# Kernel tuning notes

Hardware: AMD Instinct MI355X
Metric: run time of the kernel (lower is better)

## Reference

```python
import jax, jax.numpy as jnp
import numpy as np
from jax import lax

GROUPS = 32
CH = 2048
CG = CH // GROUPS  # 64 channels per group
H = W = 64
B = 4
EPS = 1e-5


def _conv2d(x, w, b, padding, dilation=1):
    # x: [N, Cin, H, W], w: [Cout, Cin, kh, kw] (OIHW)
    y = lax.conv_general_dilated(
        x, w, window_strides=(1, 1),
        padding=[(padding, padding), (padding, padding)],
        rhs_dilation=(dilation, dilation),
        dimension_numbers=("NCHW", "OIHW", "NCHW"))
    return y + b[None, :, None, None]


def _prelu(x, alpha):
    # single shared slope (num_parameters=1)
    return jnp.where(x >= 0, x, alpha[0] * x)


def setup_inputs() -> dict:
    key = jax.random.key(0)
    ks = jax.random.split(key, 6)
    s = 0.05
    f32 = jnp.float32
    return {
        "x": jax.random.normal(ks[0], (B, CH, H, W), f32),
        # EFFM.conv1x1 (on concatenated pooled h/w strips)
        "w_hw": jax.random.normal(ks[1], (CG, CG, 1, 1), f32) * s,
        "b_hw": jnp.zeros((CG,), f32),
        # GroupNorm(cg, cg): per-channel affine
        "gn_w": jnp.ones((CG,), f32),
        "gn_b": jnp.zeros((CG,), f32),
        # RC branch1: 3x3 conv pad=1 + PReLU
        "w_b1": jax.random.normal(ks[2], (CG, CG, 3, 3), f32) * s,
        "b_b1": jnp.zeros((CG,), f32),
        "a_b1": jnp.full((1,), 0.25, f32),
        # RC branch2: 3x3 conv dilation=2 pad=2 + PReLU
        "w_b2": jax.random.normal(ks[3], (CG, CG, 3, 3), f32) * s,
        "b_b2": jnp.zeros((CG,), f32),
        "a_b2": jnp.full((1,), 0.25, f32),
        # RC conv128to64: 1x1 conv 2*cg -> cg
        "w_cat": jax.random.normal(ks[4], (CG, 2 * CG, 1, 1), f32) * s,
        "b_cat": jnp.zeros((CG,), f32),
    }


def _effm(x, w_hw, b_hw, gn_w, gn_b, w_b1, b_b1, a_b1, w_b2, b_b2, a_b2, w_cat, b_cat):
    b, c, h, w = x.shape
    cg = c // GROUPS
    bg = b * GROUPS
    gx = x.reshape(bg, cg, h, w)

    # --- coordinate attention branch ---
    x_h = jnp.mean(gx, axis=3, keepdims=True)                       # [bg, cg, h, 1]
    x_w = jnp.mean(gx, axis=2, keepdims=True).transpose(0, 1, 3, 2)  # [bg, cg, w, 1]
    hw = jnp.concatenate([x_h, x_w], axis=2)                         # [bg, cg, h+w, 1]
    # 1x1 conv == channel mixing linear
    hw = jnp.einsum("oi,bilk->bolk", w_hw[:, :, 0, 0], hw) + b_hw[None, :, None, None]
    x_h, x_w = hw[:, :, :h, :], hw[:, :, h:, :]
    gate = gx * jax.nn.sigmoid(x_h) * jax.nn.sigmoid(x_w.transpose(0, 1, 3, 2))

    # GroupNorm(num_groups=cg, num_channels=cg) == per-channel instance norm
    mu = jnp.mean(gate, axis=(2, 3), keepdims=True)
    var = jnp.var(gate, axis=(2, 3), keepdims=True)
    x1 = (gate - mu) * lax.rsqrt(var + EPS)
    x1 = x1 * gn_w[None, :, None, None] + gn_b[None, :, None, None]

    # --- RC multi-scale branch ---
    br1 = _prelu(_conv2d(gx, w_b1, b_b1, padding=1), a_b1) + gx
    br2 = _prelu(_conv2d(gx, w_b2, b_b2, padding=2, dilation=2), a_b2) + gx
    cat = jnp.concatenate([br1, br2], axis=1)                        # [bg, 2cg, h, w]
    x2 = jnp.einsum("oi,bihw->bohw", w_cat[:, :, 0, 0], cat) + b_cat[None, :, None, None]

    # --- cross softmax-matmul attention ---
    x11 = jax.nn.softmax(jnp.mean(x1, axis=(2, 3)), axis=-1)          # [bg, cg]
    x21 = jax.nn.softmax(jnp.mean(x2, axis=(2, 3)), axis=-1)          # [bg, cg]
    weights = (jnp.einsum("gc,gchw->ghw", x11, x2)
               + jnp.einsum("gc,gchw->ghw", x21, x1))                # [bg, h, w]
    out = gx * jax.nn.sigmoid(weights)[:, None, :, :]
    return out.reshape(b, c, h, w)


def reference(x, w_hw, b_hw, gn_w, gn_b, w_b1, b_b1, a_b1, w_b2, b_b2, a_b2, w_cat, b_cat):
    return _effm(x, w_hw, b_hw, gn_w, gn_b, w_b1, b_b1, a_b1, w_b2, b_b2, a_b2, w_cat, b_cat)
```

## Files before the change

### kernel.cpp

```cpp
#include <hip/hip_runtime.h>
#include <hip/hip_bf16.h>

#define HWPX 4096

typedef __attribute__((ext_vector_type(8))) short short8v;
typedef __attribute__((ext_vector_type(4))) float f32x4;
typedef __attribute__((ext_vector_type(16))) float f32x16;
#define MFMA32(a,b,c) __builtin_amdgcn_mfma_f32_32x32x16_bf16(a,b,c,0,0,0)

__device__ __forceinline__ float sigf(float x){ return 1.0f/(1.0f+__expf(-x)); }
__device__ __forceinline__ unsigned short f2bf(float f){
  __hip_bfloat16 h = __float2bfloat16(f);
  unsigned short u; __builtin_memcpy(&u, &h, sizeof(u)); return u;
}
__device__ __forceinline__ float bf2f(unsigned short u){
  return __uint_as_float(((unsigned)u)<<16);
}
__device__ __forceinline__ void gl2lds16(const void* g, void* l){
  __builtin_amdgcn_global_load_lds((const __attribute__((address_space(1))) void*)g,
                                   (__attribute__((address_space(3))) void*)l, 16, 0, 0);
}

__global__ __launch_bounds__(256) void k_prep(const float* wb1, const float* wb2,
                                              const float* wcat, const float* gnb,
                                              unsigned short* wimg, unsigned short* wcimg,
                                              float* x11){
  int bid = blockIdx.x, tid = threadIdx.x;
  for (int idx = bid*256 + tid; idx < 73728; idx += 64*256){
    int f = idx >> 9, r = idx & 511, lane = r >> 3, j = r & 7;
    int qc = f / 36, rem = f % 36, tap = rem >> 2, kc = rem & 3;
    int q = qc >> 1, conv = qc & 1, kf = kc >> 1, cot = kc & 1;
    int co = cot*32 + (lane & 31);
    int ci = q*32 + kf*16 + (lane >> 5)*8 + j;
    const float* src = conv ? wb2 : wb1;
    wimg[idx] = f2bf(src[(co*64 + ci)*9 + tap]);
  }
  if (bid == 0){
    for (int idx = tid; idx < 8192; idx += 256){
      int f = idx >> 9, r = idx & 511, lane = r >> 3, j = r & 7;
      int kfc = f >> 1, cot = f & 1;
      int o = cot*32 + (lane & 31);
      int ch = kfc*16 + (lane >> 5)*8 + j;
      wcimg[idx] = f2bf(wcat[o*128 + ch]);
    }
    if (tid < 64){
      float g = gnb[tid];
      float m = g;
      for (int s=32; s; s>>=1) m = fmaxf(m, __shfl_xor(m, s));
      float e = __expf(g-m);
      float se = e;
      for (int s=32; s; s>>=1) se += __shfl_xor(se, s);
      x11[tid] = e/se;
    }
  }
}

__global__ __launch_bounds__(256) void k_rc(const float* __restrict__ x,
                                            unsigned short* __restrict__ xb,
                                            float* __restrict__ hwbuf){
  int blk = blockIdx.x;
  int g = blk >> 3, slot = blk & 7;
  int tid = threadIdx.x;
  int col = tid & 63, wid = tid >> 6;
  __shared__ float rsm[8*64];
  __shared__ float csm[4*8*64];
  float colacc[8] = {0,0,0,0,0,0,0,0};
  const float* xbase = x + ((size_t)(g*64 + slot*8))*HWPX;
  for (int p=0;p<16;++p){
    int r = wid + 4*p;
    const float* src = xbase + r*64 + col;
    float v[8];
    #pragma unroll
    for (int e=0;e<8;e++) v[e] = src[(size_t)e*HWPX];
    unsigned pk[4];
    #pragma unroll
    for (int j=0;j<4;j++) pk[j] = (unsigned)f2bf(v[2*j]) | ((unsigned)f2bf(v[2*j+1])<<16);
    f32x4 st; __builtin_memcpy(&st, pk, 16);
    *(f32x4*)((char*)xb + (((size_t)(g*64+r))*8 + slot)*1024 + col*16) = st;
    #pragma unroll
    for (int e=0;e<8;e++){
      float s = v[e];
      s += __shfl_xor(s,1); s += __shfl_xor(s,2); s += __shfl_xor(s,4);
      s += __shfl_xor(s,8); s += __shfl_xor(s,16); s += __shfl_xor(s,32);
      if ((tid&63)==0) rsm[e*64+r] = s;
      colacc[e] += v[e];
    }
  }
  #pragma unroll
  for (int e=0;e<8;e++) csm[(wid*8+e)*64+col] = colacc[e];
  __syncthreads();
  float* hb = hwbuf + ((size_t)(g*64 + slot*8))*128;
  for (int idx=tid; idx<512; idx+=256){
    int e = idx>>6, r = idx&63;
    hb[e*128 + r] = rsm[e*64+r] * (1.0f/64.0f);
  }
  for (int idx=tid; idx<512; idx+=256){
    int e = idx>>6, c2 = idx&63;
    float s = csm[(0*8+e)*64+c2] + csm[(1*8+e)*64+c2] + csm[(2*8+e)*64+c2] + csm[(3*8+e)*64+c2];
    hb[e*128 + 64 + c2] = s * (1.0f/64.0f);
  }
}

__global__ __launch_bounds__(256) void k_hwmm(const float* hwbuf, const float* whw,
                                              const float* bhw, float* sigbuf){
  int g = blockIdx.x;
  __shared__ float hl[64*128];
  int tid = threadIdx.x;
  const float* src = hwbuf + (size_t)g*8192;
  for (int i = tid; i < 2048; i += 256) ((float4*)hl)[i] = ((const float4*)src)[i];
  __syncthreads();
  int p  = tid & 127;
  int o0 = (tid >> 7) * 32;
  float acc[32];
  #pragma unroll
  for (int k=0;k<32;k++) acc[k] = bhw[o0+k];
  for (int i=0;i<64;i++){
    float v = hl[i*128+p];
    #pragma unroll
    for (int k=0;k<32;k++) acc[k] = fmaf(whw[(o0+k)*64+i], v, acc[k]);
  }
  float* dst = sigbuf + (size_t)g*8192;
  #pragma unroll
  for (int k=0;k<32;k++) dst[(o0+k)*128+p] = sigf(acc[k]);
}

__global__ __launch_bounds__(256) void k_gate2(const unsigned short* __restrict__ xb,
                                               const float* __restrict__ sigbuf,
                                               const float* __restrict__ gnw,
                                               const float* __restrict__ gnb,
                                               float* __restrict__ scsh){
  int blk = blockIdx.x;
  int g = blk >> 3, slot = blk & 7;
  int tid = threadIdx.x, col = tid & 63, wq = tid >> 6, lane = tid & 63;
  __shared__ float srm[8*64], scm[8*64], red[4*16];
  for (int idx = tid; idx < 1024; idx += 256){
    int e = idx >> 7, k = idx & 127;
    float v = sigbuf[(size_t)g*8192 + (size_t)(slot*8+e)*128 + k];
    if (k < 64) srm[e*64+k] = v; else scm[e*64+k-64] = v;
  }
  __syncthreads();
  float s[8] = {0,0,0,0,0,0,0,0}, s2[8] = {0,0,0,0,0,0,0,0};
  const char* base = (const char*)xb + (((size_t)(g*64))*8 + slot)*1024;
  for (int p=0;p<16;++p){
    int row = wq*16 + p;
    short8v xv = *(const short8v*)(base + (size_t)row*8192 + col*16);
    #pragma unroll
    for (int e=0;e<8;e++){
      float v = bf2f((unsigned short)xv[e]) * srm[e*64+row] * scm[e*64+col];
      s[e] += v; s2[e] = fmaf(v, v, s2[e]);
    }
  }
  #pragma unroll
  for (int e=0;e<8;e++){
    #pragma unroll
    for (int off=1; off<64; off<<=1){ s[e] += __shfl_xor(s[e], off); s2[e] += __shfl_xor(s2[e], off); }
  }
  if (lane == 0){
    #pragma unroll
    for (int e=0;e<8;e++){ red[wq*16+e] = s[e]; red[wq*16+8+e] = s2[e]; }
  }
  __syncthreads();
  if (tid < 8){
    float S  = red[tid]   + red[16+tid] + red[32+tid] + red[48+tid];
    float S2 = red[8+tid] + red[24+tid] + red[40+tid] + red[56+tid];
    float mu = S*(1.f/4096.f);
    float var = S2*(1.f/4096.f) - mu*mu;
    int c = slot*8 + tid;
    float scale = rsqrtf(var + 1e-5f) * gnw[c];
    scsh[(g*64+c)*2]   = scale;
    scsh[(g*64+c)*2+1] = gnb[c] - mu*scale;
  }
}

__global__ __launch_bounds__(512) void k_convcat(const unsigned short* __restrict__ xb,
                                                 const char* __restrict__ wgl,
                                                 const char* __restrict__ wcgl,
                                                 const float* __restrict__ bb1,
                                                 const float* __restrict__ bb2,
                                                 const float* __restrict__ a1p,
                                                 const float* __restrict__ a2p,
                                                 const float* __restrict__ bcat,
                                                 const float* __restrict__ x11,
                                                 float* __restrict__ wsum2,
                                                 float* __restrict__ x2mean){
  extern __shared__ char smem[];
  char* INL = smem;
  char* WL  = smem + 52224;
  char* BRL = smem;
  char* WCL = smem + 131072;
  float* x11l = (float*)(smem + 147456);
  float* bcl  = x11l + 64;

  const int tid = threadIdx.x;
  const int g = blockIdx.x >> 3;
  const int strip = blockIdx.x & 7;
  const int r0 = strip*8;
  const int w = tid >> 6;
  const int lane = tid & 63;
  const int l31 = lane & 31;
  const int lh  = lane >> 5;
  const int conv = w >> 2;
  const int ch2 = (w >> 1) & 1;
  const int rquad = w & 1;
  const int dil = conv + 1;

  #pragma unroll
  for (int k=0;k<2;k++){
    int idx = tid + k*512;
    gl2lds16(wcgl + (size_t)idx*16, WCL + idx*16);
  }
  if (tid < 64){ x11l[tid] = x11[tid]; bcl[tid] = bcat[tid]; }
  if (tid < 192){
    int seg = tid >> 2, pc = tid & 3;
    int colp = (pc < 2) ? pc : pc + 64;
    *(f32x4*)(INL + seg*1088 + colp*16) = (f32x4){0.f,0.f,0.f,0.f};
  }

  f32x16 acc[2][4];
  #pragma unroll
  for (int cot=0;cot<2;cot++)
    #pragma unroll
    for (int pt=0;pt<4;pt++)
      #pragma unroll
      for (int e=0;e<16;e++) acc[cot][pt][e] = 0.f;

  const float alpha = conv ? a2p[0] : a1p[0];
  const float* bbp = conv ? bb2 : bb1;

  for (int q=0;q<2;++q){
    if (q) __syncthreads();
    #pragma unroll
    for (int k=0;k<9;k++){
      int idx = tid + k*512;
      gl2lds16(wgl + (size_t)q*73728 + (size_t)idx*16, WL + idx*16);
    }
    #pragma unroll
    for (int i=0;i<6;++i){
      int seg = w*6 + i;
      int row = seg >> 2, slot = seg & 3;
      int rg = r0 - 2 + row;
      char* dst = INL + seg*1088 + 32;
      if ((unsigned)rg < 64u){
        const char* src = (const char*)xb + ((((size_t)(g*64+rg))*8) + q*4 + slot)*1024 + lane*16;
        gl2lds16(src, dst + lane*16);
      } else {
        *(f32x4*)(dst + lane*16) = (f32x4){0.f,0.f,0.f,0.f};
      }
    }
    __syncthreads();
    #pragma unroll
    for (int tap=0;tap<9;++tap){
      const int dy = tap/3 - 1, dx = tap%3 - 1;
      #pragma unroll
      for (int kf=0;kf<2;++kf){
        const char* wp = WL + (size_t)(((conv*9+tap)*4 + kf*2)*1024) + lane*16;
        short8v A0 = *(const short8v*)(wp);
        short8v A1 = *(const short8v*)(wp + 1024);
        const char* ib = INL + (kf*2 + lh)*1088 + (ch2*32 + 2 + l31 + dx*dil)*16;
        #pragma unroll
        for (int pt=0;pt<4;++pt){
          int rowin = rquad*4 + pt + dy*dil + 2;
          short8v B = *(const short8v*)(ib + rowin*4352);
          acc[0][pt] = MFMA32(A0, B, acc[0][pt]);
          acc[1][pt] = MFMA32(A1, B, acc[1][pt]);
        }
      }
    }
  }
  __syncthreads();

  #pragma unroll
  for (int cot=0;cot<2;++cot){
    #pragma unroll
    for (int rq=0;rq<4;++rq){
      int co0 = cot*32 + 8*rq + 4*lh;
      float b0 = bbp[co0], b1 = bbp[co0+1], b2 = bbp[co0+2], b3 = bbp[co0+3];
      int ch0 = conv*64 + co0;
      #pragma unroll
      for (int pt=0;pt<4;++pt){
        int prow = rquad*4 + pt;
        int colg = ch2*32 + l31;
        const char* rsrc = (const char*)xb + (((size_t)(g*64 + r0 + prow))*8 + (co0>>3))*1024
                           + colg*16 + (co0&7)*2;
        ushort4 rv = *(const ushort4*)rsrc;
        float v0 = acc[cot][pt][rq*4+0] + b0; v0 = (v0>=0.f? v0 : alpha*v0) + bf2f(rv.x);
        float v1 = acc[cot][pt][rq*4+1] + b1; v1 = (v1>=0.f? v1 : alpha*v1) + bf2f(rv.y);
        float v2 = acc[cot][pt][rq*4+2] + b2; v2 = (v2>=0.f? v2 : alpha*v2) + bf2f(rv.z);
        float v3 = acc[cot][pt][rq*4+3] + b3; v3 = (v3>=0.f? v3 : alpha*v3) + bf2f(rv.w);
        int px = prow*64 + colg;
        int addr = (px*256 + ch0*2) ^ ((px & 15) << 4);
        ushort4 pk; pk.x=f2bf(v0); pk.y=f2bf(v1); pk.z=f2bf(v2); pk.w=f2bf(v3);
        *(ushort4*)(BRL + addr) = pk;
      }
    }
  }
  __syncthreads();

  {
    f32x16 c2[2][2];
    #pragma unroll
    for (int cot=0;cot<2;cot++)
      #pragma unroll
      for (int t=0;t<2;t++)
        #pragma unroll
        for (int e=0;e<16;e++) c2[cot][t][e] = 0.f;

    #pragma unroll
    for (int kfc=0;kfc<8;++kfc){
      const char* ap = WCL + (size_t)(kfc*2*1024) + lane*16;
      short8v A0 = *(const short8v*)(ap);
      short8v A1 = *(const short8v*)(ap + 1024);
      #pragma unroll
      for (int t=0;t<2;++t){
        int px = w*64 + t*32 + l31;
        int addr = (px*256 + kfc*32 + lh*16) ^ ((px & 15) << 4);
        short8v B = *(const short8v*)(BRL + addr);
        c2[0][t] = MFMA32(A0, B, c2[0][t]);
        c2[1][t] = MFMA32(A1, B, c2[1][t]);
      }
    }
    float u0 = 0.f, u1 = 0.f;
    #pragma unroll
    for (int cot=0;cot<2;++cot){
      #pragma unroll
      for (int reg=0;reg<16;++reg){
        int o = cot*32 + (reg&3) + 8*(reg>>2) + 4*lh;
        float xw = x11l[o], bc = bcl[o];
        u0 += xw*(c2[cot][0][reg] + bc);
        u1 += xw*(c2[cot][1][reg] + bc);
        float sv = c2[cot][0][reg] + c2[cot][1][reg];
        sv += __shfl_xor(sv, 1); sv += __shfl_xor(sv, 2);
        sv += __shfl_xor(sv, 4); sv += __shfl_xor(sv, 8); sv += __shfl_xor(sv, 16);
        if (l31 == 0) atomicAdd(&x2mean[g*64 + o], sv);
      }
    }
    u0 += __shfl_xor(u0, 32);
    u1 += __shfl_xor(u1, 32);
    if (lh == 0){
      float* wp2 = wsum2 + (size_t)g*4096 + strip*512 + w*64 + l31;
      wp2[0]  = u0;
      wp2[32] = u1;
    }
  }
}

__global__ __launch_bounds__(64) void k_x21s(const float* x2mean, const float* bcat, float* x21){
  int g = blockIdx.x;
  int o = threadIdx.x;
  float mean = x2mean[g*64 + o] * (1.f/4096.f) + bcat[o];
  float mx = mean;
  for (int s=32; s; s>>=1) mx = fmaxf(mx, __shfl_xor(mx, s));
  float e = __expf(mean - mx);
  float se = e;
  for (int s=32; s; s>>=1) se += __shfl_xor(se, s);
  x21[g*64 + o] = e/se;
}

__global__ __launch_bounds__(256) void k_final(const float* __restrict__ x,
                                               const float* __restrict__ sigbuf,
                                               const float* __restrict__ scsh,
                                               const float* __restrict__ x21,
                                               const float* __restrict__ wsum2,
                                               float* __restrict__ out){
  int blk = blockIdx.x;
  int g = blk >> 4, chunk = blk & 15;
  int tid = threadIdx.x;
  __shared__ float crow[64*4];
  __shared__ float ccol[64*64];
  __shared__ float Ssm;
  const float* sgb = sigbuf + (size_t)g*8192;
  {
    int c = tid >> 2, rr = tid & 3;
    crow[tid] = x21[g*64+c] * scsh[(g*64+c)*2] * sgb[c*128 + chunk*4 + rr];
  }
  for (int idx = tid; idx < 4096; idx += 256){
    int c = idx >> 6, col = idx & 63;
    ccol[idx] = sgb[c*128 + 64 + col];
  }
  if (tid < 64){
    float v = x21[g*64+tid] * scsh[(g*64+tid)*2+1];
    for (int s=32; s; s>>=1) v += __shfl_xor(v, s);
    if (tid == 0) Ssm = v;
  }
  __syncthreads();
  int px = chunk*256 + tid;
  int rr = tid >> 6, col = tid & 63;
  const float* xp = x + (size_t)(g*64)*HWPX + px;
  float W = wsum2[(size_t)g*4096 + px] + Ssm;
  #pragma unroll 4
  for (int c=0;c<64;c++){
    W = fmaf(crow[c*4+rr]*ccol[c*64+col], xp[(size_t)c*HWPX], W);
  }
  float s = sigf(W);
  float* op = out + (size_t)(g*64)*HWPX + px;
  #pragma unroll 4
  for (int c=0;c<64;c++){
    op[(size_t)c*HWPX] = xp[(size_t)c*HWPX] * s;
  }
}

extern "C" void kernel_launch(void* const* d_in, const int* in_sizes, int n_in,
                              void* d_out, int out_size, void* d_ws, size_t ws_size,
                              hipStream_t stream) {
  const float* x     = (const float*)d_in[0];
  const float* w_hw  = (const float*)d_in[1];
  const float* b_hw  = (const float*)d_in[2];
  const float* gn_w  = (const float*)d_in[3];
  const float* gn_b  = (const float*)d_in[4];
  const float* w_b1  = (const float*)d_in[5];
  const float* b_b1  = (const float*)d_in[6];
  const float* a_b1  = (const float*)d_in[7];
  const float* w_b2  = (const float*)d_in[8];
  const float* b_b2  = (const float*)d_in[9];
  const float* a_b2  = (const float*)d_in[10];
  const float* w_cat = (const float*)d_in[11];
  const float* b_cat = (const float*)d_in[12];

  char* ws = (char*)d_ws;
  unsigned short* wimg  = (unsigned short*)(ws + 0);
  unsigned short* wcimg = (unsigned short*)(ws + 147456);
  float* x11    = (float*)(ws + 163840);
  float* x21    = (float*)(ws + 164096);
  float* x2mean = (float*)(ws + 196864);
  float* scsh   = (float*)(ws + 229632);
  float* wsum2  = (float*)(ws + 295168);
  float* hwbuf  = (float*)(ws + 2392320);
  float* sigb   = (float*)(ws + 6586624);
  unsigned short* xb = (unsigned short*)d_out;
  float* out = (float*)d_out;

  hipFuncSetAttribute(reinterpret_cast<const void*>(k_convcat),
                      hipFuncAttributeMaxDynamicSharedMemorySize, 147968);

  k_prep <<<64,   256, 0, stream>>>(w_b1, w_b2, w_cat, gn_b, wimg, wcimg, x11);
  k_rc   <<<1024, 256, 0, stream>>>(x, xb, hwbuf);
  k_hwmm <<<128,  256, 0, stream>>>(hwbuf, w_hw, b_hw, sigb);
  k_gate2<<<1024, 256, 0, stream>>>(xb, sigb, gn_w, gn_b, scsh);
  hipMemsetAsync(x2mean, 0, 32768, stream);
  k_convcat<<<1024, 512, 147968, stream>>>(xb, (const char*)wimg, (const char*)wcimg,
                                           b_b1, b_b2, a_b1, a_b2, b_cat, x11, wsum2, x2mean);
  k_x21s <<<128,  64, 0, stream>>>(x2mean, b_cat, x21);
  k_final<<<2048, 256, 0, stream>>>(x, sigb, scsh, x21, wsum2, out);
}
```

Baseline: 298.4 us.

## Merge prep/rc/memset launches, restructure convcat staging, fuse x21 softmax into final

The weight-prep, x-cast/pooling and x2mean zeroing kernels are folded into one launch, and the x21 softmax kernel is folded into the final kernel, removing several launches and a memset. In convcat, the per-half weight staging into LDS is dropped: weights and cat weights are read straight from global memory, and both input halves are double-buffered in LDS so the second half's load overlaps the first half's MFMA work. The conv loop is templated on dilation, and input rows are loaded into registers once per column offset and reused across taps. Block-index swizzles are added to gate2 and convcat, and the final kernel keeps x in registers to avoid reading it twice. The cost is more global and L2 traffic for the weight reads and higher register pressure.

New measurement: 303.4 us. About the same (+1.7%).

```diff
diff --git a/kernel.cpp b/kernel.cpp
--- a/kernel.cpp
+++ b/kernel.cpp
@@ -21,46 +21,57 @@
                                    (__attribute__((address_space(3))) void*)l, 16, 0, 0);
 }
 
-__global__ __launch_bounds__(256) void k_prep(const float* wb1, const float* wb2,
-                                              const float* wcat, const float* gnb,
-                                              unsigned short* wimg, unsigned short* wcimg,
-                                              float* x11){
+__global__ __launch_bounds__(256) void k_pre(const float* __restrict__ x,
+                                             const float* __restrict__ wb1,
+                                             const float* __restrict__ wb2,
+                                             const float* __restrict__ wcat,
+                                             const float* __restrict__ gnb,
+                                             unsigned short* __restrict__ xb,
+                                             float* __restrict__ hwbuf,
+                                             unsigned short* __restrict__ wimg,
+                                             unsigned short* __restrict__ wcimg,
+                                             float* __restrict__ x11,
+                                             float* __restrict__ x2mean){
   int bid = blockIdx.x, tid = threadIdx.x;
-  for (int idx = bid*256 + tid; idx < 73728; idx += 64*256){
-    int f = idx >> 9, r = idx & 511, lane = r >> 3, j = r & 7;
-    int qc = f / 36, rem = f % 36, tap = rem >> 2, kc = rem & 3;
-    int q = qc >> 1, conv = qc & 1, kf = kc >> 1, cot = kc & 1;
-    int co = cot*32 + (lane & 31);
-    int ci = q*32 + kf*16 + (lane >> 5)*8 + j;
-    const float* src = conv ? wb2 : wb1;
-    wimg[idx] = f2bf(src[(co*64 + ci)*9 + tap]);
-  }
-  if (bid == 0){
-    for (int idx = tid; idx < 8192; idx += 256){
+  if (bid >= 1088){
+    int idx = (bid - 1088)*2048 + tid*8;
+    f32x4 z = {0.f,0.f,0.f,0.f};
+    *(f32x4*)(x2mean + idx) = z;
+    *(f32x4*)(x2mean + idx + 4) = z;
+    return;
+  }
+  if (bid >= 1024){
+    int bid2 = bid - 1024;
+    for (int idx = bid2*256 + tid; idx < 73728; idx += 64*256){
       int f = idx >> 9, r = idx & 511, lane = r >> 3, j = r & 7;
-      int kfc = f >> 1, cot = f & 1;
-      int o = cot*32 + (lane & 31);
-      int ch = kfc*16 + (lane >> 5)*8 + j;
-      wcimg[idx] = f2bf(wcat[o*128 + ch]);
-    }
-    if (tid < 64){
-      float g = gnb[tid];
-      float m = g;
-      for (int s=32; s; s>>=1) m = fmaxf(m, __shfl_xor(m, s));
-      float e = __expf(g-m);
-      float se = e;
-      for (int s=32; s; s>>=1) se += __shfl_xor(se, s);
-      x11[tid] = e/se;
-    }
-  }
-}
-
-__global__ __launch_bounds__(256) void k_rc(const float* __restrict__ x,
-                                            unsigned short* __restrict__ xb,
-                                            float* __restrict__ hwbuf){
-  int blk = blockIdx.x;
-  int g = blk >> 3, slot = blk & 7;
-  int tid = threadIdx.x;
+      int qc = f / 36, rem = f % 36, tap = rem >> 2, kc = rem & 3;
+      int q = qc >> 1, conv = qc & 1, kf = kc >> 1, cot = kc & 1;
+      int co = cot*32 + (lane & 31);
+      int ci = q*32 + kf*16 + (lane >> 5)*8 + j;
+      const float* src = conv ? wb2 : wb1;
+      wimg[idx] = f2bf(src[(co*64 + ci)*9 + tap]);
+    }
+    if (bid2 == 0){
+      for (int idx = tid; idx < 8192; idx += 256){
+        int f = idx >> 9, r = idx & 511, lane = r >> 3, j = r & 7;
+        int kfc = f >> 1, cot = f & 1;
+        int o = cot*32 + (lane & 31);
+        int ch = kfc*16 + (lane >> 5)*8 + j;
+        wcimg[idx] = f2bf(wcat[o*128 + ch]);
+      }
+      if (tid < 64){
+        float g = gnb[tid];
+        float m = g;
+        for (int s=32; s; s>>=1) m = fmaxf(m, __shfl_xor(m, s));
+        float e = __expf(g-m);
+        float se = e;
+        for (int s=32; s; s>>=1) se += __shfl_xor(se, s);
+        x11[tid] = e/se;
+      }
+    }
+    return;
+  }
+  int g = bid >> 3, slot = bid & 7;
   int col = tid & 63, wid = tid >> 6;
   __shared__ float rsm[8*64];
   __shared__ float csm[4*8*64];
@@ -129,8 +140,8 @@
                                                const float* __restrict__ gnw,
                                                const float* __restrict__ gnb,
                                                float* __restrict__ scsh){
-  int blk = blockIdx.x;
-  int g = blk >> 3, slot = blk & 7;
+  int bsw = (blockIdx.x & 7)*(gridDim.x >> 3) + (blockIdx.x >> 3);
+  int g = bsw >> 3, slot = bsw & 7;
   int tid = threadIdx.x, col = tid & 63, wq = tid >> 6, lane = tid & 63;
   __shared__ float srm[8*64], scm[8*64], red[4*16];
   for (int idx = tid; idx < 1024; idx += 256){
@@ -169,6 +180,38 @@
     float scale = rsqrtf(var + 1e-5f) * gnw[c];
     scsh[(g*64+c)*2]   = scale;
     scsh[(g*64+c)*2+1] = gnb[c] - mu*scale;
+  }
+}
+
+template<int DIL>
+__device__ __forceinline__ void conv_compute(const char* INq, const char* wq,
+                                             int ch2, int rquad, int l31, int lh, int lane,
+                                             f32x16 acc[2][4]){
+  constexpr int NROW = 4 + 2*DIL;
+  #pragma unroll
+  for (int kf=0; kf<2; ++kf){
+    #pragma unroll
+    for (int dxx=0; dxx<3; ++dxx){
+      const int colb = ch2*32 + l31 + (dxx-1)*DIL + 2;
+      short8v Brow[NROW];
+      #pragma unroll
+      for (int i=0; i<NROW; ++i){
+        int rowi = rquad*4 + i + 2 - DIL;
+        Brow[i] = *(const short8v*)(INq + (rowi*4 + kf*2 + lh)*1088 + colb*16);
+      }
+      #pragma unroll
+      for (int dyy=0; dyy<3; ++dyy){
+        int tap = dyy*3 + dxx;
+        const char* wp = wq + (size_t)(tap*4 + kf*2)*1024 + lane*16;
+        short8v A0 = *(const short8v*)(wp);
+        short8v A1 = *(const short8v*)(wp + 1024);
+        #pragma unroll
+        for (int pt=0; pt<4; ++pt){
+          acc[0][pt] = MFMA32(A0, Brow[pt + dyy*DIL], acc[0][pt]);
+          acc[1][pt] = MFMA32(A1, Brow[pt + dyy*DIL], acc[1][pt]);
+        }
+      }
+    }
   }
 }
 
@@ -184,16 +227,14 @@
                                                  float* __restrict__ wsum2,
                                                  float* __restrict__ x2mean){
   extern __shared__ char smem[];
-  char* INL = smem;
-  char* WL  = smem + 52224;
   char* BRL = smem;
-  char* WCL = smem + 131072;
-  float* x11l = (float*)(smem + 147456);
+  float* x11l = (float*)(smem + 131072);
   float* bcl  = x11l + 64;
 
   const int tid = threadIdx.x;
-  const int g = blockIdx.x >> 3;
-  const int strip = blockIdx.x & 7;
+  const int bsw = (blockIdx.x & 7)*(gridDim.x >> 3) + (blockIdx.x >> 3);
+  const int g = bsw >> 3;
+  const int strip = bsw & 7;
   const int r0 = strip*8;
   const int w = tid >> 6;
   const int lane = tid & 63;
@@ -202,18 +243,27 @@
   const int conv = w >> 2;
   const int ch2 = (w >> 1) & 1;
   const int rquad = w & 1;
-  const int dil = conv + 1;
-
-  #pragma unroll
-  for (int k=0;k<2;k++){
-    int idx = tid + k*512;
-    gl2lds16(wcgl + (size_t)idx*16, WCL + idx*16);
-  }
+
   if (tid < 64){ x11l[tid] = x11[tid]; bcl[tid] = bcat[tid]; }
-  if (tid < 192){
-    int seg = tid >> 2, pc = tid & 3;
+  if (tid < 384){
+    int b = tid / 192, t = tid % 192;
+    int seg = t >> 2, pc = t & 3;
     int colp = (pc < 2) ? pc : pc + 64;
-    *(f32x4*)(INL + seg*1088 + colp*16) = (f32x4){0.f,0.f,0.f,0.f};
+    *(f32x4*)(smem + b*52224 + seg*1088 + colp*16) = (f32x4){0.f,0.f,0.f,0.f};
+  }
+
+  #pragma unroll
+  for (int i=0;i<6;++i){
+    int seg = w*6 + i;
+    int row = seg >> 2, slot = seg & 3;
+    int rg = r0 - 2 + row;
+    char* dst = smem + seg*1088 + 32;
+    if ((unsigned)rg < 64u){
+      const char* src = (const char*)xb + ((((size_t)(g*64+rg))*8) + slot)*1024 + lane*16;
+      gl2lds16(src, dst + lane*16);
+    } else {
+      *(f32x4*)(dst + lane*16) = (f32x4){0.f,0.f,0.f,0.f};
+    }
   }
 
   f32x16 acc[2][4];
@@ -224,73 +274,62 @@
       #pragma unroll
       for (int e=0;e<16;e++) acc[cot][pt][e] = 0.f;
 
-  const float alpha = conv ? a2p[0] : a1p[0];
-  const float* bbp = conv ? bb2 : bb1;
-
-  for (int q=0;q<2;++q){
-    if (q) __syncthreads();
-    #pragma unroll
-    for (int k=0;k<9;k++){
-      int idx = tid + k*512;
-      gl2lds16(wgl + (size_t)q*73728 + (size_t)idx*16, WL + idx*16);
-    }
-    #pragma unroll
-    for (int i=0;i<6;++i){
-      int seg = w*6 + i;
-      int row = seg >> 2, slot = seg & 3;
-      int rg = r0 - 2 + row;
-      char* dst = INL + seg*1088 + 32;
-      if ((unsigned)rg < 64u){
-        const char* src = (const char*)xb + ((((size_t)(g*64+rg))*8) + q*4 + slot)*1024 + lane*16;
-        gl2lds16(src, dst + lane*16);
-      } else {
-        *(f32x4*)(dst + lane*16) = (f32x4){0.f,0.f,0.f,0.f};
-      }
-    }
-    __syncthreads();
-    #pragma unroll
-    for (int tap=0;tap<9;++tap){
-      const int dy = tap/3 - 1, dx = tap%3 - 1;
-      #pragma unroll
-      for (int kf=0;kf<2;++kf){
-        const char* wp = WL + (size_t)(((conv*9+tap)*4 + kf*2)*1024) + lane*16;
-        short8v A0 = *(const short8v*)(wp);
-        short8v A1 = *(const short8v*)(wp + 1024);
-        const char* ib = INL + (kf*2 + lh)*1088 + (ch2*32 + 2 + l31 + dx*dil)*16;
+  __syncthreads();
+
+  #pragma unroll
+  for (int i=0;i<6;++i){
+    int seg = w*6 + i;
+    int row = seg >> 2, slot = seg & 3;
+    int rg = r0 - 2 + row;
+    char* dst = smem + 52224 + seg*1088 + 32;
+    if ((unsigned)rg < 64u){
+      const char* src = (const char*)xb + ((((size_t)(g*64+rg))*8) + 4 + slot)*1024 + lane*16;
+      gl2lds16(src, dst + lane*16);
+    } else {
+      *(f32x4*)(dst + lane*16) = (f32x4){0.f,0.f,0.f,0.f};
+    }
+  }
+
+  {
+    const char* wq = wgl + (size_t)((0*2 + conv)*9*4)*1024;
+    if (conv == 0) conv_compute<1>(smem, wq, ch2, rquad, l31, lh, lane, acc);
+    else           conv_compute<2>(smem, wq, ch2, rquad, l31, lh, lane, acc);
+  }
+  __syncthreads();
+
+  {
+    const char* wq = wgl + (size_t)((1*2 + conv)*9*4)*1024;
+    if (conv == 0) conv_compute<1>(smem + 52224, wq, ch2, rquad, l31, lh, lane, acc);
+    else           conv_compute<2>(smem + 52224, wq, ch2, rquad, l31, lh, lane, acc);
+  }
+  __syncthreads();
+
+  {
+    const float alpha = conv ? a2p[0] : a1p[0];
+    const float* bbp = conv ? bb2 : bb1;
+    #pragma unroll
+    for (int cot=0;cot<2;++cot){
+      #pragma unroll
+      for (int rq=0;rq<4;++rq){
+        int co0 = cot*32 + 8*rq + 4*lh;
+        float b0 = bbp[co0], b1 = bbp[co0+1], b2 = bbp[co0+2], b3 = bbp[co0+3];
+        int ch0 = conv*64 + co0;
         #pragma unroll
         for (int pt=0;pt<4;++pt){
-          int rowin = rquad*4 + pt + dy*dil + 2;
-          short8v B = *(const short8v*)(ib + rowin*4352);
-          acc[0][pt] = MFMA32(A0, B, acc[0][pt]);
-          acc[1][pt] = MFMA32(A1, B, acc[1][pt]);
+          int prow = rquad*4 + pt;
+          int colg = ch2*32 + l31;
+          const char* rsrc = (const char*)xb + (((size_t)(g*64 + r0 + prow))*8 + (co0>>3))*1024
+                             + colg*16 + (co0&7)*2;
+          ushort4 rv = *(const ushort4*)rsrc;
+          float v0 = acc[cot][pt][rq*4+0] + b0; v0 = (v0>=0.f? v0 : alpha*v0) + bf2f(rv.x);
+          float v1 = acc[cot][pt][rq*4+1] + b1; v1 = (v1>=0.f? v1 : alpha*v1) + bf2f(rv.y);
+          float v2 = acc[cot][pt][rq*4+2] + b2; v2 = (v2>=0.f? v2 : alpha*v2) + bf2f(rv.z);
+          float v3 = acc[cot][pt][rq*4+3] + b3; v3 = (v3>=0.f? v3 : alpha*v3) + bf2f(rv.w);
+          int px = prow*64 + colg;
+          int addr = (px*256 + ch0*2) ^ ((px & 15) << 4);
+          ushort4 pk; pk.x=f2bf(v0); pk.y=f2bf(v1); pk.z=f2bf(v2); pk.w=f2bf(v3);
+          *(ushort4*)(BRL + addr) = pk;
         }
-      }
-    }
-  }
-  __syncthreads();
-
-  #pragma unroll
-  for (int cot=0;cot<2;++cot){
-    #pragma unroll
-    for (int rq=0;rq<4;++rq){
-      int co0 = cot*32 + 8*rq + 4*lh;
-      float b0 = bbp[co0], b1 = bbp[co0+1], b2 = bbp[co0+2], b3 = bbp[co0+3];
-      int ch0 = conv*64 + co0;
-      #pragma unroll
-      for (int pt=0;pt<4;++pt){
-        int prow = rquad*4 + pt;
-        int colg = ch2*32 + l31;
-        const char* rsrc = (const char*)xb + (((size_t)(g*64 + r0 + prow))*8 + (co0>>3))*1024
-                           + colg*16 + (co0&7)*2;
-        ushort4 rv = *(const ushort4*)rsrc;
-        float v0 = acc[cot][pt][rq*4+0] + b0; v0 = (v0>=0.f? v0 : alpha*v0) + bf2f(rv.x);
-        float v1 = acc[cot][pt][rq*4+1] + b1; v1 = (v1>=0.f? v1 : alpha*v1) + bf2f(rv.y);
-        float v2 = acc[cot][pt][rq*4+2] + b2; v2 = (v2>=0.f? v2 : alpha*v2) + bf2f(rv.z);
-        float v3 = acc[cot][pt][rq*4+3] + b3; v3 = (v3>=0.f? v3 : alpha*v3) + bf2f(rv.w);
-        int px = prow*64 + colg;
-        int addr = (px*256 + ch0*2) ^ ((px & 15) << 4);
-        ushort4 pk; pk.x=f2bf(v0); pk.y=f2bf(v1); pk.z=f2bf(v2); pk.w=f2bf(v3);
-        *(ushort4*)(BRL + addr) = pk;
       }
     }
   }
@@ -307,7 +346,7 @@
 
     #pragma unroll
     for (int kfc=0;kfc<8;++kfc){
-      const char* ap = WCL + (size_t)(kfc*2*1024) + lane*16;
+      const char* ap = wcgl + (size_t)(kfc*2)*1024 + lane*16;
       short8v A0 = *(const short8v*)(ap);
       short8v A1 = *(const short8v*)(ap + 1024);
       #pragma unroll
@@ -344,41 +383,41 @@
   }
 }
 
-__global__ __launch_bounds__(64) void k_x21s(const float* x2mean, const float* bcat, float* x21){
-  int g = blockIdx.x;
-  int o = threadIdx.x;
-  float mean = x2mean[g*64 + o] * (1.f/4096.f) + bcat[o];
-  float mx = mean;
-  for (int s=32; s; s>>=1) mx = fmaxf(mx, __shfl_xor(mx, s));
-  float e = __expf(mean - mx);
-  float se = e;
-  for (int s=32; s; s>>=1) se += __shfl_xor(se, s);
-  x21[g*64 + o] = e/se;
-}
-
-__global__ __launch_bounds__(256) void k_final(const float* __restrict__ x,
-                                               const float* __restrict__ sigbuf,
-                                               const float* __restrict__ scsh,
-                                               const float* __restrict__ x21,
-                                               const float* __restrict__ wsum2,
-                                               float* __restrict__ out){
+__global__ __launch_bounds__(256) void k_final2(const float* __restrict__ x,
+                                                const float* __restrict__ sigbuf,
+                                                const float* __restrict__ scsh,
+                                                const float* __restrict__ x2mean,
+                                                const float* __restrict__ bcat,
+                                                const float* __restrict__ wsum2,
+                                                float* __restrict__ out){
   int blk = blockIdx.x;
   int g = blk >> 4, chunk = blk & 15;
   int tid = threadIdx.x;
+  __shared__ float x21s[64];
   __shared__ float crow[64*4];
   __shared__ float ccol[64*64];
   __shared__ float Ssm;
   const float* sgb = sigbuf + (size_t)g*8192;
-  {
-    int c = tid >> 2, rr = tid & 3;
-    crow[tid] = x21[g*64+c] * scsh[(g*64+c)*2] * sgb[c*128 + chunk*4 + rr];
+  if (tid < 64){
+    float mean = x2mean[g*64 + tid] * (1.f/4096.f) + bcat[tid];
+    float mx = mean;
+    for (int s=32; s; s>>=1) mx = fmaxf(mx, __shfl_xor(mx, s));
+    float e = __expf(mean - mx);
+    float se = e;
+    for (int s=32; s; s>>=1) se += __shfl_xor(se, s);
+    x21s[tid] = e/se;
   }
   for (int idx = tid; idx < 4096; idx += 256){
     int c = idx >> 6, col = idx & 63;
     ccol[idx] = sgb[c*128 + 64 + col];
   }
+  __syncthreads();
+  {
+    int c = tid >> 2, rr = tid & 3;
+    crow[tid] = x21s[c] * scsh[(g*64+c)*2] * sgb[c*128 + chunk*4 + rr];
+  }
   if (tid < 64){
-    float v = x21[g*64+tid] * scsh[(g*64+tid)*2+1];
+    float v = x21s[tid] * scsh[(g*64+tid)*2+1];
     for (int s=32; s; s>>=1) v += __shfl_xor(v, s);
     if (tid == 0) Ssm = v;
   }
@@ -387,15 +426,17 @@
   int rr = tid >> 6, col = tid & 63;
   const float* xp = x + (size_t)(g*64)*HWPX + px;
   float W = wsum2[(size_t)g*4096 + px] + Ssm;
-  #pragma unroll 4
+  float xv[64];
+  #pragma unroll
   for (int c=0;c<64;c++){
-    W = fmaf(crow[c*4+rr]*ccol[c*64+col], xp[(size_t)c*HWPX], W);
+    xv[c] = xp[(size_t)c*HWPX];
+    W = fmaf(crow[c*4+rr]*ccol[c*64+col], xv[c], W);
   }
   float s = sigf(W);
   float* op = out + (size_t)(g*64)*HWPX + px;
-  #pragma unroll 4
+  #pragma unroll
   for (int c=0;c<64;c++){
-    op[(size_t)c*HWPX] = xp[(size_t)c*HWPX] * s;
+    op[(size_t)c*HWPX] = xv[c] * s;
   }
 }
 
@@ -420,25 +461,22 @@
   unsigned short* wimg  = (unsigned short*)(ws + 0);
   unsigned short* wcimg = (unsigned short*)(ws + 147456);
   float* x11    = (float*)(ws + 163840);
-  float* x21    = (float*)(ws + 164096);
-  float* x2mean = (float*)(ws + 196864);
-  float* scsh   = (float*)(ws + 229632);
-  float* wsum2  = (float*)(ws + 295168);
-  float* hwbuf  = (float*)(ws + 2392320);
-  float* sigb   = (float*)(ws + 6586624);
+  float* x2mean = (float*)(ws + 164096);
+  float* scsh   = (float*)(ws + 196864);
+  float* wsum2  = (float*)(ws + 262400);
+  float* hwbuf  = (float*)(ws + 2359552);
+  float* sigb   = (float*)(ws + 6553856);
   unsigned short* xb = (unsigned short*)d_out;
   float* out = (float*)d_out;
 
   hipFuncSetAttribute(reinterpret_cast<const void*>(k_convcat),
-                      hipFuncAttributeMaxDynamicSharedMemorySize, 147968);
-
-  k_prep <<<64,   256, 0, stream>>>(w_b1, w_b2, w_cat, gn_b, wimg, wcimg, x11);
-  k_rc   <<<1024, 256, 0, stream>>>(x, xb, hwbuf);
+                      hipFuncAttributeMaxDynamicSharedMemorySize, 131584);
+
+  k_pre  <<<1092, 256, 0, stream>>>(x, w_b1, w_b2, w_cat, gn_b, xb, hwbuf, wimg, wcimg,
+                                    x11, x2mean);
   k_hwmm <<<128,  256, 0, stream>>>(hwbuf, w_hw, b_hw, sigb);
   k_gate2<<<1024, 256, 0, stream>>>(xb, sigb, gn_w, gn_b, scsh);
-  hipMemsetAsync(x2mean, 0, 32768, stream);
-  k_convcat<<<1024, 512, 147968, stream>>>(xb, (const char*)wimg, (const char*)wcimg,
+  k_convcat<<<1024, 512, 131584, stream>>>(xb, (const char*)wimg, (const char*)wcimg,
                                            b_b1, b_b2, a_b1, a_b2, b_cat, x11, wsum2, x2mean);
-  k_x21s <<<128,  64, 0, stream>>>(x2mean, b_cat, x21);
-  k_final<<<2048, 256, 0, stream>>>(x, sigb, scsh, x21, wsum2, out);
-}
+  k_final2<<<2048, 256, 0, stream>>>(x, sigb, scsh, x2mean, b_cat, wsum2, out);
+}
```
